# Performance work log

Hardware: AMD Instinct MI355X
Metric: run time of the kernel (lower is better)

Reference implementation:

```python
import jax, jax.numpy as jnp
import numpy as np

B, CIN, COUT, T, S = 4, 32, 64, 8, 3   # batch, in-ch, out-ch, num_taps, stencil edge
D, H, W = 32, 64, 64                    # input volume
PAD = 1                                 # zero padding (stride 1) -> same spatial output


def setup_inputs() -> dict:
    key = jax.random.key(0)
    k1, k2, k3, k4 = jax.random.split(key, 4)
    x = jax.random.normal(k1, (B, CIN, D, H, W), jnp.float32)
    stencils = jax.random.normal(k2, (B, T, S, S, S), jnp.float32)
    weight = jax.random.normal(k3, (COUT, CIN, T), jnp.float32) * 0.05
    bias = jax.random.normal(k4, (COUT,), jnp.float32) * 0.05
    return {"x": x, "stencils": stencils, "weight": weight, "bias": bias}


def reference(x, stencils, weight, bias):
    # x: (B,Cin,D,H,W); stencils: (B,T,sx,sy,sz); weight: (Cout,Cin,T); bias: (Cout,)
    b, cin = x.shape[:2]
    t = stencils.shape[1]
    sx, sy, sz = stencils.shape[2:]
    # zero-pad spatially
    xp = jnp.pad(x, ((0, 0), (0, 0), (PAD, PAD), (PAD, PAD), (PAD, PAD)))
    # fold batch into channels -> grouped conv with groups = B*Cin (per-sample stencils)
    x_exp = xp.reshape(1, b * cin, xp.shape[2], xp.shape[3], xp.shape[4])
    # per-sample stencils shared across Cin, one output feature per (b, cin, tap)
    w = jnp.broadcast_to(stencils[:, None], (b, cin, t, sx, sy, sz))
    w = w.reshape(b * cin * t, 1, sx, sy, sz)
    tap = jax.lax.conv_general_dilated(
        x_exp, w,
        window_strides=(1, 1, 1), padding='VALID',
        dimension_numbers=('NCDHW', 'OIDHW', 'NCDHW'),
        feature_group_count=b * cin,
    )  # (1, B*Cin*T, Do, Ho, Wo)
    do, ho, wo = tap.shape[-3:]
    tap = tap.reshape(b, cin, t, do, ho, wo)
    # channel/tap mixing: (B,Cin,T,D,H,W) x (Cout,Cin,T) -> (B,Cout,D,H,W)
    y = jnp.einsum('bctdhw,oct->bodhw', tap, weight)
    return y + bias[None, :, None, None, None]
```

## Files before the change

### kernel.cpp

```cpp
#include <hip/hip_runtime.h>

typedef short bf16x8 __attribute__((ext_vector_type(8)));
typedef float f32x16 __attribute__((ext_vector_type(16)));

#define XROW 2176

__device__ __forceinline__ unsigned short f2bf(float f) {
    unsigned u = __float_as_uint(f);
    return (unsigned short)((u + 0x7FFFu + ((u >> 16) & 1u)) >> 16);
}

__global__ __launch_bounds__(256) void prep_keff(const float* __restrict__ stencils,
                                                 const float* __restrict__ weight,
                                                 uint4* __restrict__ kf2) {
    int i = blockIdx.x * 256 + threadIdx.x;
    if (i >= 27648) return;
    int lane = i & 63;
    int mt = (i >> 6) & 1;
    int s  = (i >> 7) & 1;
    int br = i >> 8;
    int r = br % 27, b = br / 27;
    int o  = (lane & 31) + 32 * mt;
    int cb = s * 16 + (lane >> 5) * 8;
    float st[8];
    #pragma unroll
    for (int t = 0; t < 8; ++t) st[t] = stencils[((size_t)b * 8 + t) * 27 + r];
    unsigned short us[8];
    #pragma unroll
    for (int j = 0; j < 8; ++j) {
        const float* wp = weight + ((size_t)o * 32 + cb + j) * 8;
        float acc = 0.f;
        #pragma unroll
        for (int t = 0; t < 8; ++t) acc += wp[t] * st[t];
        us[j] = f2bf(acc);
    }
    uint4 v;
    v.x = us[0] | ((unsigned)us[1] << 16);
    v.y = us[2] | ((unsigned)us[3] << 16);
    v.z = us[4] | ((unsigned)us[5] << 16);
    v.w = us[6] | ((unsigned)us[7] << 16);
    kf2[i] = v;
}

__global__ __launch_bounds__(256, 2) void conv_fused(
    const float* __restrict__ x, const uint4* __restrict__ kf2,
    const float* __restrict__ bias, float* __restrict__ out) {
    __shared__ __align__(1024) char smem[52224];

    int n = blockIdx.x;
    int xcd = n & 7, local = n >> 3;
    int dt = local & 15;
    int cmb = (local >> 4) | (xcd << 4);
    int ht = cmb & 15, wt = (cmb >> 4) & 1, b = cmb >> 5;

    int tid = threadIdx.x;
    int lane = tid & 63, wid = tid >> 6;
    int nlo = lane & 31, kh = lane >> 5;

    for (int task = tid; task < 3264; task += 256) {
        int row = task / 136;
        int chunk = task - row * 136;
        int q = chunk & 3, xp = chunk >> 2;
        int z = row / 6, yy = row - z * 6;
        int gd = dt * 2 + z - 1, gh = ht * 4 + yy - 1, gw = wt * 32 + xp - 1;
        uint4 v = make_uint4(0u, 0u, 0u, 0u);
        if ((unsigned)gd < 32u && (unsigned)gh < 64u && (unsigned)gw < 64u) {
            const float* xb = x + (((size_t)(b * 32 + q * 8) * 32 + gd) * 64 + gh) * 64 + gw;
            unsigned short us[8];
            #pragma unroll
            for (int j = 0; j < 8; ++j)
                us[j] = f2bf(xb[(size_t)j * 131072]);
            v.x = us[0] | ((unsigned)us[1] << 16);
            v.y = us[2] | ((unsigned)us[3] << 16);
            v.z = us[4] | ((unsigned)us[5] << 16);
            v.w = us[6] | ((unsigned)us[7] << 16);
        }
        int pos = q ^ ((xp >> 1) & 3);
        *(uint4*)(smem + row * XROW + xp * 64 + (pos << 4)) = v;
    }

    int z = wid >> 1;
    int ys = (wid & 1) << 1;

    int Badr[2][3];
    #pragma unroll
    for (int s = 0; s < 2; ++s)
        #pragma unroll
        for (int k3 = 0; k3 < 3; ++k3) {
            int xl = nlo + k3;
            int pos = (s * 2 + kh) ^ ((xl >> 1) & 3);
            Badr[s][k3] = (z * 6 + ys) * XROW + xl * 64 + (pos << 4);
        }

    const uint4* kfb = kf2 + (size_t)b * 27 * 256 + lane;

    bf16x8 aCur[4], aNxt[4];
    #pragma unroll
    for (int fi = 0; fi < 4; ++fi)
        aCur[fi] = *(const bf16x8*)(kfb + fi * 64);

    f32x16 acc[2][2];
    #pragma unroll
    for (int mt = 0; mt < 2; ++mt)
        #pragma unroll
        for (int nt = 0; nt < 2; ++nt)
            #pragma unroll
            for (int e = 0; e < 16; ++e) acc[mt][nt][e] = 0.f;

    __syncthreads();

    #pragma unroll
    for (int r = 0; r < 27; ++r) {
        const int i3 = r / 9, j3 = (r / 3) % 3, k3 = r % 3;
        if (r < 26) {
            #pragma unroll
            for (int fi = 0; fi < 4; ++fi)
                aNxt[fi] = *(const bf16x8*)(kfb + ((r + 1) * 4 + fi) * 64);
        }
        #pragma unroll
        for (int s = 0; s < 2; ++s) {
            #pragma unroll
            for (int nt = 0; nt < 2; ++nt) {
                bf16x8 bb = *(const bf16x8*)(smem + (i3 * 6 + j3 + nt) * XROW + Badr[s][k3]);
                acc[0][nt] = __builtin_amdgcn_mfma_f32_32x32x16_bf16(aCur[s * 2 + 0], bb, acc[0][nt], 0, 0, 0);
                acc[1][nt] = __builtin_amdgcn_mfma_f32_32x32x16_bf16(aCur[s * 2 + 1], bb, acc[1][nt], 0, 0, 0);
            }
        }
        if (r < 26) {
            #pragma unroll
            for (int fi = 0; fi < 4; ++fi) aCur[fi] = aNxt[fi];
        }
    }

    int d = dt * 2 + z, w = wt * 32 + nlo;
    #pragma unroll
    for (int mt = 0; mt < 2; ++mt) {
        #pragma unroll
        for (int nt = 0; nt < 2; ++nt) {
            int h = ht * 4 + ys + nt;
            size_t sp = (((size_t)d) * 64 + h) * 64 + w;
            #pragma unroll
            for (int reg = 0; reg < 16; ++reg) {
                int o = mt * 32 + (reg & 3) + 8 * (reg >> 2) + 4 * kh;
                out[(((size_t)(b * 64 + o)) << 17) + sp] = acc[mt][nt][reg] + bias[o];
            }
        }
    }
}

extern "C" void kernel_launch(void* const* d_in, const int* in_sizes, int n_in,
                              void* d_out, int out_size, void* d_ws, size_t ws_size,
                              hipStream_t stream) {
    const float* x        = (const float*)d_in[0];
    const float* stencils = (const float*)d_in[1];
    const float* weight   = (const float*)d_in[2];
    const float* bias     = (const float*)d_in[3];
    float* out = (float*)d_out;

    uint4* kf2 = (uint4*)d_ws;

    prep_keff<<<108, 256, 0, stream>>>(stencils, weight, kf2);
    conv_fused<<<2048, 256, 0, stream>>>(x, kf2, bias, out);
}
```

Baseline: 250.3 us.

## Pre-transpose input to padded bf16 layout and stream tiles via global_load_lds

A prep pass converts x once into a zero-padded, channel-interleaved, swizzled bf16 buffer in workspace. The conv kernel then copies each tile straight into LDS with async global_load_lds, with no per-element conversion or bounds checks, and targets 3 blocks per CU. The halo re-reads of strided fp32 data and the conversion work inside the conv are removed. In exchange there is an extra ~38MB write and read pass through HBM, plus a fallback path when the workspace is too small.

```diff
diff --git a/kernel.cpp b/kernel.cpp
--- a/kernel.cpp
+++ b/kernel.cpp
@@ -4,45 +4,187 @@
 typedef float f32x16 __attribute__((ext_vector_type(16)));
 
 #define XROW 2176
+#define KF2_BYTES 442368
+#define XT_ROWS 8976
+#define XT_ROW_BYTES 4224
+#define XT_BYTES 37914624
+#define WS_NEED (KF2_BYTES + XT_BYTES)
 
 __device__ __forceinline__ unsigned short f2bf(float f) {
     unsigned u = __float_as_uint(f);
     return (unsigned short)((u + 0x7FFFu + ((u >> 16) & 1u)) >> 16);
 }
 
-__global__ __launch_bounds__(256) void prep_keff(const float* __restrict__ stencils,
-                                                 const float* __restrict__ weight,
-                                                 uint4* __restrict__ kf2) {
-    int i = blockIdx.x * 256 + threadIdx.x;
-    if (i >= 27648) return;
-    int lane = i & 63;
-    int mt = (i >> 6) & 1;
-    int s  = (i >> 7) & 1;
-    int br = i >> 8;
-    int r = br % 27, b = br / 27;
-    int o  = (lane & 31) + 32 * mt;
-    int cb = s * 16 + (lane >> 5) * 8;
-    float st[8];
-    #pragma unroll
-    for (int t = 0; t < 8; ++t) st[t] = stencils[((size_t)b * 8 + t) * 27 + r];
+__global__ __launch_bounds__(256) void prep(const float* __restrict__ x,
+                                            const float* __restrict__ stencils,
+                                            const float* __restrict__ weight,
+                                            uint4* __restrict__ kf2,
+                                            uint4* __restrict__ xt,
+                                            int nxt) {
+    int tid = threadIdx.x;
+    int blk = blockIdx.x;
+
+    if (blk >= nxt) {
+        int i = (blk - nxt) * 256 + tid;
+        if (i >= 27648) return;
+        int lane = i & 63;
+        int mt = (i >> 6) & 1;
+        int s  = (i >> 7) & 1;
+        int br = i >> 8;
+        int r = br % 27, b = br / 27;
+        int o  = (lane & 31) + 32 * mt;
+        int cb = s * 16 + (lane >> 5) * 8;
+        float st[8];
+        #pragma unroll
+        for (int t = 0; t < 8; ++t) st[t] = stencils[((size_t)b * 8 + t) * 27 + r];
+        unsigned short us[8];
+        #pragma unroll
+        for (int j = 0; j < 8; ++j) {
+            const float* wp = weight + ((size_t)o * 32 + cb + j) * 8;
+            float acc = 0.f;
+            #pragma unroll
+            for (int t = 0; t < 8; ++t) acc += wp[t] * st[t];
+            us[j] = f2bf(acc);
+        }
+        uint4 v;
+        v.x = us[0] | ((unsigned)us[1] << 16);
+        v.y = us[2] | ((unsigned)us[3] << 16);
+        v.z = us[4] | ((unsigned)us[5] << 16);
+        v.w = us[6] | ((unsigned)us[7] << 16);
+        kf2[i] = v;
+        return;
+    }
+
+    int n = blk;
+    int ph = n % 66;
+    int t2 = n / 66;
+    int pd = t2 % 34, b = t2 / 34;
+    uint4* rowp = xt + (size_t)n * 264;
+    int d = pd - 1, h = ph - 1;
+
+    if ((unsigned)d >= 32u || (unsigned)h >= 64u) {
+        for (int i = tid; i < 264; i += 256) rowp[i] = make_uint4(0u, 0u, 0u, 0u);
+        return;
+    }
+
+    int q = tid >> 6, w = tid & 63;
+    const float* xb = x + (((size_t)(b * 32 + q * 8) * 32 + d) * 64 + h) * 64 + w;
     unsigned short us[8];
     #pragma unroll
-    for (int j = 0; j < 8; ++j) {
-        const float* wp = weight + ((size_t)o * 32 + cb + j) * 8;
-        float acc = 0.f;
-        #pragma unroll
-        for (int t = 0; t < 8; ++t) acc += wp[t] * st[t];
-        us[j] = f2bf(acc);
-    }
+    for (int j = 0; j < 8; ++j) us[j] = f2bf(xb[(size_t)j * 131072]);
     uint4 v;
     v.x = us[0] | ((unsigned)us[1] << 16);
     v.y = us[2] | ((unsigned)us[3] << 16);
     v.z = us[4] | ((unsigned)us[5] << 16);
     v.w = us[6] | ((unsigned)us[7] << 16);
-    kf2[i] = v;
-}
-
-__global__ __launch_bounds__(256, 2) void conv_fused(
+    int pw = w + 1;
+    int pos = q ^ ((pw >> 1) & 3);
+    rowp[pw * 4 + pos] = v;
+    if (tid < 4)      rowp[tid]       = make_uint4(0u, 0u, 0u, 0u);
+    else if (tid < 8) rowp[256 + tid] = make_uint4(0u, 0u, 0u, 0u);
+}
+
+__global__ __launch_bounds__(256, 3) void conv_fused(
+    const uint4* __restrict__ xt, const uint4* __restrict__ kf2,
+    const float* __restrict__ bias, float* __restrict__ out) {
+    __shared__ __align__(1024) char smem[52224];
+
+    int n = blockIdx.x;
+    int xcd = n & 7, local = n >> 3;
+    int dt = local & 15;
+    int cmb = (local >> 4) | (xcd << 4);
+    int ht = cmb & 15, wt = (cmb >> 4) & 1, b = cmb >> 5;
+
+    int tid = threadIdx.x;
+    int lane = tid & 63, wid = tid >> 6;
+    int nlo = lane & 31, kh = lane >> 5;
+
+    const uint4* kfb = kf2 + (size_t)b * 6912 + lane;
+    bf16x8 aCur[4], aNxt[4];
+    #pragma unroll
+    for (int fi = 0; fi < 4; ++fi)
+        aCur[fi] = *(const bf16x8*)(kfb + fi * 64);
+
+    const char* xtb = (const char*)xt + (size_t)b * 9478656
+                    + ((size_t)(dt * 2) * 66 + ht * 4) * XT_ROW_BYTES + wt * 2048;
+    #pragma unroll
+    for (int it = 0; it < 13; ++it) {
+        int task = tid + it * 256;
+        if (task < 3264) {
+            int row  = task / 136;
+            int cidx = task - row * 136;
+            int zz = row / 6, yy = row - zz * 6;
+            const char* gp = xtb + (zz * 66 + yy) * XT_ROW_BYTES + cidx * 16;
+            __builtin_amdgcn_global_load_lds(
+                (const __attribute__((address_space(1))) void*)gp,
+                (__attribute__((address_space(3))) void*)(smem + task * 16),
+                16, 0, 0);
+        }
+    }
+
+    int z = wid >> 1;
+    int ys = (wid & 1) << 1;
+
+    int Badr[2][3];
+    #pragma unroll
+    for (int s = 0; s < 2; ++s)
+        #pragma unroll
+        for (int k3 = 0; k3 < 3; ++k3) {
+            int xl = nlo + k3;
+            int pos = (s * 2 + kh) ^ ((xl >> 1) & 3);
+            Badr[s][k3] = (z * 6 + ys) * XROW + xl * 64 + (pos << 4);
+        }
+
+    f32x16 acc[2][2];
+    #pragma unroll
+    for (int mt = 0; mt < 2; ++mt)
+        #pragma unroll
+        for (int nt = 0; nt < 2; ++nt)
+            #pragma unroll
+            for (int e = 0; e < 16; ++e) acc[mt][nt][e] = 0.f;
+
+    __syncthreads();
+
+    #pragma unroll
+    for (int r = 0; r < 27; ++r) {
+        const int i3 = r / 9, j3 = (r / 3) % 3, k3 = r % 3;
+        if (r < 26) {
+            #pragma unroll
+            for (int fi = 0; fi < 4; ++fi)
+                aNxt[fi] = *(const bf16x8*)(kfb + ((r + 1) * 4 + fi) * 64);
+        }
+        #pragma unroll
+        for (int s = 0; s < 2; ++s) {
+            #pragma unroll
+            for (int nt = 0; nt < 2; ++nt) {
+                bf16x8 bb = *(const bf16x8*)(smem + (i3 * 6 + j3 + nt) * XROW + Badr[s][k3]);
+                acc[0][nt] = __builtin_amdgcn_mfma_f32_32x32x16_bf16(aCur[s * 2 + 0], bb, acc[0][nt], 0, 0, 0);
+                acc[1][nt] = __builtin_amdgcn_mfma_f32_32x32x16_bf16(aCur[s * 2 + 1], bb, acc[1][nt], 0, 0, 0);
+            }
+        }
+        if (r < 26) {
+            #pragma unroll
+            for (int fi = 0; fi < 4; ++fi) aCur[fi] = aNxt[fi];
+        }
+    }
+
+    int d = dt * 2 + z, w = wt * 32 + nlo;
+    #pragma unroll
+    for (int mt = 0; mt < 2; ++mt) {
+        #pragma unroll
+        for (int nt = 0; nt < 2; ++nt) {
+            int h = ht * 4 + ys + nt;
+            size_t sp = (((size_t)d) * 64 + h) * 64 + w;
+            #pragma unroll
+            for (int reg = 0; reg < 16; ++reg) {
+                int o = mt * 32 + (reg & 3) + 8 * (reg >> 2) + 4 * kh;
+                out[(((size_t)(b * 64 + o)) << 17) + sp] = acc[mt][nt][reg] + bias[o];
+            }
+        }
+    }
+}
+
+__global__ __launch_bounds__(256, 2) void conv_fused_fb(
     const float* __restrict__ x, const uint4* __restrict__ kf2,
     const float* __restrict__ bias, float* __restrict__ out) {
     __shared__ __align__(1024) char smem[52224];
@@ -92,7 +234,7 @@
             Badr[s][k3] = (z * 6 + ys) * XROW + xl * 64 + (pos << 4);
         }
 
-    const uint4* kfb = kf2 + (size_t)b * 27 * 256 + lane;
+    const uint4* kfb = kf2 + (size_t)b * 6912 + lane;
 
     bf16x8 aCur[4], aNxt[4];
     #pragma unroll
@@ -159,6 +301,12 @@
 
     uint4* kf2 = (uint4*)d_ws;
 
-    prep_keff<<<108, 256, 0, stream>>>(stencils, weight, kf2);
-    conv_fused<<<2048, 256, 0, stream>>>(x, kf2, bias, out);
-}
+    if (ws_size >= (size_t)WS_NEED) {
+        uint4* xt = (uint4*)((char*)d_ws + KF2_BYTES);
+        prep<<<XT_ROWS + 108, 256, 0, stream>>>(x, stencils, weight, kf2, xt, XT_ROWS);
+        conv_fused<<<2048, 256, 0, stream>>>(xt, kf2, bias, out);
+    } else {
+        prep<<<108, 256, 0, stream>>>(x, stencils, weight, kf2, kf2, 0);
+        conv_fused_fb<<<2048, 256, 0, stream>>>(x, kf2, bias, out);
+    }
+}
```

After: 246.4 us. About the same (-1.6%).
